# Kernel optimization log

Measured on AMD Instinct MI355X. Metric: run time of the kernel, lower is better.

## Reference

```python
import jax, jax.numpy as jnp
import numpy as np

N_HEADS = 16
EPS = 1e-4


def setup_inputs() -> dict:
    key = jax.random.key(0)
    ks = jax.random.split(key, 9)
    B, L, E = 4, 4096, 1024
    s = 1.0 / np.sqrt(E)
    return {
        "x": jax.random.normal(ks[0], (B, L, E), dtype=jnp.float32),
        "Wq": jax.random.normal(ks[1], (E, E), dtype=jnp.float32) * s,
        "bq": jax.random.normal(ks[2], (E,), dtype=jnp.float32) * 0.01,
        "Wk": jax.random.normal(ks[3], (E, E), dtype=jnp.float32) * s,
        "bk": jax.random.normal(ks[4], (E,), dtype=jnp.float32) * 0.01,
        "Wv": jax.random.normal(ks[5], (E, E), dtype=jnp.float32) * s,
        "bv": jax.random.normal(ks[6], (E,), dtype=jnp.float32) * 0.01,
        "Wo": jax.random.normal(ks[7], (E, E), dtype=jnp.float32) * s,
        "bo": jax.random.normal(ks[8], (E,), dtype=jnp.float32) * 0.01,
    }


def _cosformer(x, Wq, bq, Wk, bk, Wv, bv, Wo, bo):
    B, L, E = x.shape
    H = N_HEADS
    hd = E // H
    # torch Linear: y = x @ W.T + b; self-attention so q=k=v source is x
    q = jax.nn.relu(jnp.einsum('ble,fe->blf', x, Wq) + bq)
    k = jax.nn.relu(jnp.einsum('ble,fe->blf', x, Wk) + bk)
    v = jnp.einsum('ble,fe->blf', x, Wv) + bv
    # (B, L, E) -> (B*H, L, hd)  [matches torch view(L, B*H, hd).transpose(0,1)]
    def split_heads(t):
        return t.reshape(B, L, H, hd).transpose(0, 2, 1, 3).reshape(B * H, L, hd)
    q, k, v = split_heads(q), split_heads(k), split_heads(v)
    m = L  # src_len == tgt_len
    idx = (np.pi / 2) * jnp.arange(1, m + 1, dtype=jnp.float32) / m  # (m,)
    sin = jnp.sin(idx)[None, :, None]
    cos = jnp.cos(idx)[None, :, None]
    q_ = jnp.concatenate([q * sin, q * cos], axis=-1)  # (BH, L, 2hd)
    k_ = jnp.concatenate([k * sin, k * cos], axis=-1)
    kv = jnp.einsum('nld,nlm->ndm', k_, v)             # (BH, 2hd, hd)
    z = 1.0 / jnp.maximum(jnp.einsum('nld,nd->nl', q_, k_.sum(axis=1)), EPS)
    attn = jnp.einsum('nld,ndm->nlm', q_, kv) * z[:, :, None]  # (BH, L, hd)
    # (B*H, L, hd) -> (B, L, E)
    out = attn.reshape(B, H, L, hd).transpose(0, 2, 1, 3).reshape(B, L, E)
    return jnp.einsum('ble,fe->blf', out, Wo) + bo


def reference(x, Wq, bq, Wk, bk, Wv, bv, Wo, bo):
    return _cosformer(x, Wq, bq, Wk, bk, Wv, bv, Wo, bo)
```

## Files before the change

### kernel.cpp

```cpp
#include <hip/hip_runtime.h>


typedef unsigned short u16;
typedef unsigned int u32;
typedef __attribute__((ext_vector_type(8))) __bf16 bf16x8;
typedef __attribute__((ext_vector_type(4))) float f32x4;

#define PI_HALF 1.57079632679489662f
#define EPS_Z 1e-4f

__device__ __forceinline__ u16 f32_to_bf16(float f) {
    union { float f; unsigned int u; } x; x.f = f;
    unsigned int lsb = (x.u >> 16) & 1u;
    x.u += 0x7fffu + lsb;
    return (u16)(x.u >> 16);
}
__device__ __forceinline__ float bf16_to_f32(u16 u) {
    union { float f; unsigned int u; } x; x.u = ((unsigned int)u) << 16;
    return x.f;
}

typedef __attribute__((address_space(1))) void amdgpu_global_t;
typedef __attribute__((address_space(3))) void amdgpu_lds_t;
__device__ __forceinline__ void async_load16(const u16* g, u16* l) {
    __builtin_amdgcn_global_load_lds((amdgpu_global_t*)g, (amdgpu_lds_t*)l, 16, 0, 0);
}

__global__ __launch_bounds__(256) void cvt_bf16(const float* __restrict__ in,
                                                u16* __restrict__ out, int n4) {
    int i = blockIdx.x * 256 + threadIdx.x;
    if (i >= n4) return;
    float4 f = ((const float4*)in)[i];
    ushort4 o;
    o.x = f32_to_bf16(f.x); o.y = f32_to_bf16(f.y);
    o.z = f32_to_bf16(f.z); o.w = f32_to_bf16(f.w);
    ((ushort4*)out)[i] = o;
}

__global__ __launch_bounds__(256) void cvt_w4(const float* __restrict__ w0,
                                              const float* __restrict__ w1,
                                              const float* __restrict__ w2,
                                              const float* __restrict__ w3,
                                              u16* __restrict__ wcat) {
    const float* src = (blockIdx.y == 0) ? w0 : (blockIdx.y == 1) ? w1
                     : (blockIdx.y == 2) ? w2 : w3;
    u16* dst = wcat + (size_t)blockIdx.y * 1048576;
    int i = blockIdx.x * 256 + threadIdx.x;
    float4 f = ((const float4*)src)[i];
    ushort4 o;
    o.x = f32_to_bf16(f.x); o.y = f32_to_bf16(f.y);
    o.z = f32_to_bf16(f.z); o.w = f32_to_bf16(f.w);
    ((ushort4*)dst)[i] = o;
}

__global__ __launch_bounds__(256) void gemm_qkv(const u16* __restrict__ A,
                                                const u16* __restrict__ Wcat,
                                                const float* __restrict__ bq,
                                                const float* __restrict__ bk,
                                                const float* __restrict__ bv,
                                                u16* __restrict__ qo,
                                                u16* __restrict__ ko,
                                                u16* __restrict__ vo) {
    __shared__ u16 As[128 * 32];
    __shared__ u16 Bs[128 * 32];
    const int K = 1024;
    const int tid  = threadIdx.x;
    const int wave = tid >> 6;
    const int lane = tid & 63;
    const int quad = lane >> 4;
    const int l15  = lane & 15;
    const long tileM = (long)blockIdx.x * 128;
    const long tileN = (long)blockIdx.y * 128;
    const int mat = blockIdx.y >> 3;
    const float* bias = (mat == 0) ? bq : (mat == 1) ? bk : bv;
    u16* outp = (mat == 0) ? qo : (mat == 1) ? ko : vo;
    const bool relu = (mat < 2);
    const int wm = (wave >> 1) * 64;
    const int wn = (wave & 1) * 64;
    const int s_row = wave * 32 + (lane >> 2);
    const int s_col = (lane & 3) * 8;

    const u16* gA = A    + (tileM + s_row) * (long)K + s_col;
    const u16* gB = Wcat + (tileN + s_row) * (long)K + s_col;
    u16* lA = &As[wave * 1024];
    u16* lB = &Bs[wave * 1024];

    f32x4 acc[4][4] = {};

    for (int kb = 0; kb < K; kb += 32) {
        async_load16(gA,                lA);
        async_load16(gA + 16 * (long)K, lA + 512);
        async_load16(gB,                lB);
        async_load16(gB + 16 * (long)K, lB + 512);
        gA += 32; gB += 32;
        __syncthreads();
        bf16x8 af[4], bf[4];
#pragma unroll
        for (int i = 0; i < 4; i++) {
            af[i] = *(const bf16x8*)&As[(wm + i * 16 + l15) * 32 + quad * 8];
            bf[i] = *(const bf16x8*)&Bs[(wn + i * 16 + l15) * 32 + quad * 8];
        }
#pragma unroll
        for (int i = 0; i < 4; i++)
#pragma unroll
            for (int j = 0; j < 4; j++)
                acc[i][j] = __builtin_amdgcn_mfma_f32_16x16x32_bf16(
                    af[i], bf[j], acc[i][j], 0, 0, 0);
        __syncthreads();
    }

#pragma unroll
    for (int j = 0; j < 4; j++) {
        const long n = tileN + wn + j * 16 + l15;
        const int nl = (int)n & 1023;
        const float bv_ = bias[nl];
#pragma unroll
        for (int i = 0; i < 4; i++) {
            const long m0 = tileM + wm + i * 16 + quad * 4;
#pragma unroll
            for (int r = 0; r < 4; r++) {
                float v = acc[i][j][r] + bv_;
                if (relu) v = fmaxf(v, 0.0f);
                outp[(m0 + r) * 1024 + nl] = f32_to_bf16(v);
            }
        }
    }
}

__global__ __launch_bounds__(256) void gemm_o(const u16* __restrict__ A,
                                              const u16* __restrict__ Bw,
                                              const float* __restrict__ bias,
                                              float* __restrict__ Cout,
                                              int M, int N, int K) {
    __shared__ u16 As[128 * 32];
    __shared__ u16 Bs[128 * 32];
    const int tid  = threadIdx.x;
    const int wave = tid >> 6;
    const int lane = tid & 63;
    const int quad = lane >> 4;
    const int l15  = lane & 15;
    const long tileM = (long)blockIdx.x * 128;
    const long tileN = (long)blockIdx.y * 128;
    const int wm = (wave >> 1) * 64;
    const int wn = (wave & 1) * 64;
    const int s_row = wave * 32 + (lane >> 2);
    const int s_col = (lane & 3) * 8;

    const u16* gA = A  + (tileM + s_row) * (long)K + s_col;
    const u16* gB = Bw + (tileN + s_row) * (long)K + s_col;
    u16* lA = &As[wave * 1024];
    u16* lB = &Bs[wave * 1024];

    f32x4 acc[4][4] = {};

    for (int kb = 0; kb < K; kb += 32) {
        async_load16(gA,                lA);
        async_load16(gA + 16 * (long)K, lA + 512);
        async_load16(gB,                lB);
        async_load16(gB + 16 * (long)K, lB + 512);
        gA += 32; gB += 32;
        __syncthreads();
        bf16x8 af[4], bf[4];
#pragma unroll
        for (int i = 0; i < 4; i++) {
            af[i] = *(const bf16x8*)&As[(wm + i * 16 + l15) * 32 + quad * 8];
            bf[i] = *(const bf16x8*)&Bs[(wn + i * 16 + l15) * 32 + quad * 8];
        }
#pragma unroll
        for (int i = 0; i < 4; i++)
#pragma unroll
            for (int j = 0; j < 4; j++)
                acc[i][j] = __builtin_amdgcn_mfma_f32_16x16x32_bf16(
                    af[i], bf[j], acc[i][j], 0, 0, 0);
        __syncthreads();
    }

#pragma unroll
    for (int j = 0; j < 4; j++) {
        const long n = tileN + wn + j * 16 + l15;
        const float bv = bias[n];
#pragma unroll
        for (int i = 0; i < 4; i++) {
            const long m0 = tileM + wm + i * 16 + quad * 4;
#pragma unroll
            for (int r = 0; r < 4; r++)
                Cout[(m0 + r) * (long)N + n] = acc[i][j][r] + bv;
        }
    }
}

__global__ __launch_bounds__(256) void kv_accum(const u16* __restrict__ kmat,
                                                const u16* __restrict__ vmat,
                                                u16* __restrict__ kvp,
                                                float* __restrict__ ksp) {
    __shared__ __align__(16) float ks[32][68];
    __shared__ __align__(16) float vs[32][68];
    __shared__ float scs[32], scc[32];
    const int tid = threadIdx.x;
    const int head = blockIdx.y;
    const int b = head >> 4, h = head & 15;
    const int l0 = blockIdx.x * 128;
    const int lt = tid >> 3;
    const int g  = tid & 7;
    const int dp = tid & 31;
    const int mg = tid >> 5;
    const int dk0 = dp * 2;

    float as0[8] = {}, ac0[8] = {}, as1[8] = {}, ac1[8] = {};
    float ks0s = 0.f, ks0c = 0.f, ks1s = 0.f, ks1c = 0.f;

    for (int tile = 0; tile < 4; tile++) {
        const int lbase = l0 + tile * 32;
        {
            const long row = ((long)b * 4096 + lbase + lt) * 1024 + h * 64 + g * 8;
            uint4 kk = *(const uint4*)(kmat + row);
            uint4 vv = *(const uint4*)(vmat + row);
            const u16* kp = (const u16*)&kk;
            const u16* vp = (const u16*)&vv;
#pragma unroll
            for (int j = 0; j < 8; j++) {
                ks[lt][g * 8 + j] = bf16_to_f32(kp[j]);
                vs[lt][g * 8 + j] = bf16_to_f32(vp[j]);
            }
        }
        if (tid < 32) {
            float idx = PI_HALF * (float)(lbase + tid + 1) * (1.0f / 4096.0f);
            scs[tid] = sinf(idx);
            scc[tid] = cosf(idx);
        }
        __syncthreads();
#pragma unroll 4
        for (int l = 0; l < 32; l++) {
            const float sn = scs[l], cs = scc[l];
            const float2 kk = *(const float2*)&ks[l][dk0];
            const float k0s = kk.x * sn, k0c = kk.x * cs;
            const float k1s = kk.y * sn, k1c = kk.y * cs;
            ks0s += k0s; ks0c += k0c; ks1s += k1s; ks1c += k1c;
            const float4 va = *(const float4*)&vs[l][mg * 8];
            const float4 vb = *(const float4*)&vs[l][mg * 8 + 4];
            const float vv8[8] = {va.x, va.y, va.z, va.w, vb.x, vb.y, vb.z, vb.w};
#pragma unroll
            for (int j = 0; j < 8; j++) {
                as0[j] = fmaf(k0s, vv8[j], as0[j]);
                ac0[j] = fmaf(k0c, vv8[j], ac0[j]);
                as1[j] = fmaf(k1s, vv8[j], as1[j]);
                ac1[j] = fmaf(k1c, vv8[j], ac1[j]);
            }
        }
        __syncthreads();
    }
    u16* base = kvp + ((long)blockIdx.x * 64 + head) * 8192;
#pragma unroll
    for (int j = 0; j < 8; j++) {
        u32 s01 = (u32)f32_to_bf16(as0[j]) | ((u32)f32_to_bf16(as1[j]) << 16);
        u32 c01 = (u32)f32_to_bf16(ac0[j]) | ((u32)f32_to_bf16(ac1[j]) << 16);
        *(u32*)(base + (mg * 8 + j) * 128 + dk0)      = s01;
        *(u32*)(base + (mg * 8 + j) * 128 + 64 + dk0) = c01;
    }
    if (mg == 0) {
        float* kb2 = ksp + ((long)blockIdx.x * 64 + head) * 128;
        *(float2*)(kb2 + dk0)      = make_float2(ks0s, ks1s);
        *(float2*)(kb2 + 64 + dk0) = make_float2(ks0c, ks1c);
    }
}

__global__ __launch_bounds__(256) void kv_reduce(const u16* __restrict__ kvp,
                                                 const float* __restrict__ ksp,
                                                 u16* __restrict__ Bt) {
    const int idx = blockIdx.x * 256 + threadIdx.x;
    const int d2 = idx & 127;
    const int n  = (idx >> 7) % 80;
    const int head = idx / (80 * 128);
    float s = 0.0f;
    if (n < 64) {
#pragma unroll
        for (int c = 0; c < 32; c++)
            s += bf16_to_f32(kvp[((long)c * 64 + head) * 8192 + n * 128 + d2]);
    } else if (n == 64) {
#pragma unroll
        for (int c = 0; c < 32; c++)
            s += ksp[((long)c * 64 + head) * 128 + d2];
    }
    Bt[(long)head * 10240 + n * 128 + d2] = f32_to_bf16(s);
}

__global__ __launch_bounds__(256) void attn_mfma(const u16* __restrict__ qb,
                                                 const u16* __restrict__ Bt,
                                                 u16* __restrict__ merged) {
    __shared__ __align__(16) u16 As[128 * 72];
    __shared__ __align__(16) u16 Bs[80 * 136];
    const int tid = threadIdx.x;
    const int wave = tid >> 6, lane = tid & 63;
    const int quad = lane >> 4, l15 = lane & 15;
    const int head = blockIdx.y;
    const int b = head >> 4, h = head & 15;
    const int tm = blockIdx.x * 128;
    const long b4 = (long)b * 4096;

    for (int c = tid; c < 1024; c += 256) {
        const int row = c >> 3, c8 = c & 7;
        uint4 t = *(const uint4*)(qb + (b4 + tm + row) * 1024 + h * 64 + c8 * 8);
        *(uint4*)&As[row * 72 + c8 * 8] = t;
    }
    for (int c = tid; c < 1280; c += 256) {
        const int row = c >> 4, c16 = c & 15;
        uint4 t = *(const uint4*)(Bt + (long)head * 10240 + row * 128 + c16 * 8);
        *(uint4*)&Bs[row * 136 + c16 * 8] = t;
    }
    const int wm = wave * 32;
    float snl[2], csl[2];
#pragma unroll
    for (int i = 0; i < 2; i++) {
        const int l = tm + wm + i * 16 + l15;
        const float idx = PI_HALF * (float)(l + 1) * (1.0f / 4096.0f);
        snl[i] = sinf(idx); csl[i] = cosf(idx);
    }
    __syncthreads();

    f32x4 acc[2][5] = {};
#pragma unroll
    for (int kb = 0; kb < 4; kb++) {
        const int qc = (kb & 1) * 32 + quad * 8;
        bf16x8 af[2];
#pragma unroll
        for (int i = 0; i < 2; i++) {
            bf16x8 raw = *(const bf16x8*)&As[(wm + i * 16 + l15) * 72 + qc];
            const float s = (kb < 2) ? snl[i] : csl[i];
            bf16x8 sc;
#pragma unroll
            for (int e = 0; e < 8; e++) sc[e] = (__bf16)((float)raw[e] * s);
            af[i] = sc;
        }
        bf16x8 bf[5];
#pragma unroll
        for (int j = 0; j < 5; j++)
            bf[j] = *(const bf16x8*)&Bs[(j * 16 + l15) * 136 + kb * 32 + quad * 8];
#pragma unroll
        for (int i = 0; i < 2; i++)
#pragma unroll
            for (int j = 0; j < 5; j++)
                acc[i][j] = __builtin_amdgcn_mfma_f32_16x16x32_bf16(
                    af[i], bf[j], acc[i][j], 0, 0, 0);
    }

#pragma unroll
    for (int i = 0; i < 2; i++) {
        float z[4];
#pragma unroll
        for (int r = 0; r < 4; r++) {
            const float den = __shfl(acc[i][4][r], lane & 0x30, 64);
            z[r] = 1.0f / fmaxf(den, EPS_Z);
        }
#pragma unroll
        for (int j = 0; j < 4; j++)
#pragma unroll
            for (int r = 0; r < 4; r++) {
                const int l = tm + wm + i * 16 + quad * 4 + r;
                merged[(b4 + l) * 1024 + h * 64 + j * 16 + l15] =
                    f32_to_bf16(acc[i][j][r] * z[r]);
            }
    }
}

extern "C" void kernel_launch(void* const* d_in, const int* in_sizes, int n_in,
                              void* d_out, int out_size, void* d_ws, size_t ws_size,
                              hipStream_t stream) {
    (void)in_sizes; (void)n_in; (void)out_size; (void)ws_size;
    const float* x  = (const float*)d_in[0];
    const float* Wq = (const float*)d_in[1];
    const float* bq = (const float*)d_in[2];
    const float* Wk = (const float*)d_in[3];
    const float* bk = (const float*)d_in[4];
    const float* Wv = (const float*)d_in[5];
    const float* bv = (const float*)d_in[6];
    const float* Wo = (const float*)d_in[7];
    const float* bo = (const float*)d_in[8];
    float* out = (float*)d_out;

    const int M = 16384, E = 1024;
    char* ws = (char*)d_ws;
    const size_t MB = 1048576;
    u16* xb   = (u16*)(ws);
    u16* qb   = (u16*)(ws + 32 * MB);
    u16* kb   = (u16*)(ws + 64 * MB);
    u16* vb   = (u16*)(ws + 96 * MB);
    u16* wcat = (u16*)(ws + 128 * MB);
    u16* wob  = wcat + 3 * (size_t)E * E;
    u16* Btb  = (u16*)(ws + 136 * MB);
    float* ksp = (float*)(ws + 136 * MB + 1310720 + 2048);
    u16* kvp  = xb;
    u16* mergedb = kb;

    cvt_bf16<<<dim3(M * E / 4 / 256), dim3(256), 0, stream>>>(x, xb, M * E / 4);
    cvt_w4<<<dim3(E * E / 4 / 256, 4), dim3(256), 0, stream>>>(Wq, Wk, Wv, Wo, wcat);

    gemm_qkv<<<dim3(M / 128, 24), dim3(256), 0, stream>>>(xb, wcat, bq, bk, bv,
                                                          qb, kb, vb);

    kv_accum<<<dim3(32, 64), dim3(256), 0, stream>>>(kb, vb, kvp, ksp);
    kv_reduce<<<dim3(2560), dim3(256), 0, stream>>>(kvp, ksp, Btb);
    attn_mfma<<<dim3(32, 64), dim3(256), 0, stream>>>(qb, Btb, mergedb);

    gemm_o<<<dim3(M / 128, E / 128), dim3(256), 0, stream>>>(mergedb, wob, bo,
                                                             out, M, E, E);
}
```

Measured before the change: 410.7 us.

## Compute K^T V accumulation with bf16 MFMA and fold k-sum into ones column

Replaces the scalar-FMA kv_accum kernel with an MFMA-based kernel that transposes K and V tiles into swizzled LDS, scales K by sin/cos (updated by angle-addition recurrence), and multiplies with V plus a ones column to get the k-sum at the same time. Each block now covers 512 positions instead of 128, so there are fewer partials, which are written in fp32 and reduced by a new transposing kernel through LDS. This targets the FMA-bound kv accumulation and the reduce traffic. In exchange, scaled K is rounded to bf16 before the MFMA and the sin/cos recurrence can drift.

```diff
diff --git a/kernel.cpp b/kernel.cpp
--- a/kernel.cpp
+++ b/kernel.cpp
@@ -189,99 +189,117 @@
     }
 }
 
-__global__ __launch_bounds__(256) void kv_accum(const u16* __restrict__ kmat,
-                                                const u16* __restrict__ vmat,
-                                                u16* __restrict__ kvp,
-                                                float* __restrict__ ksp) {
-    __shared__ __align__(16) float ks[32][68];
-    __shared__ __align__(16) float vs[32][68];
-    __shared__ float scs[32], scc[32];
+__global__ __launch_bounds__(256) void kv_mfma(const u16* __restrict__ kmat,
+                                               const u16* __restrict__ vmat,
+                                               float* __restrict__ part) {
+    __shared__ u16 Ak[64 * 40];
+    __shared__ u16 Bv[64 * 40];
     const int tid = threadIdx.x;
+    const int wave = tid >> 6, lane = tid & 63;
+    const int quad = lane >> 4, l15 = lane & 15;
     const int head = blockIdx.y;
     const int b = head >> 4, h = head & 15;
-    const int l0 = blockIdx.x * 128;
-    const int lt = tid >> 3;
-    const int g  = tid & 7;
-    const int dp = tid & 31;
-    const int mg = tid >> 5;
-    const int dk0 = dp * 2;
-
-    float as0[8] = {}, ac0[8] = {}, as1[8] = {}, ac1[8] = {};
-    float ks0s = 0.f, ks0c = 0.f, ks1s = 0.f, ks1c = 0.f;
-
-    for (int tile = 0; tile < 4; tile++) {
-        const int lbase = l0 + tile * 32;
-        {
-            const long row = ((long)b * 4096 + lbase + lt) * 1024 + h * 64 + g * 8;
-            uint4 kk = *(const uint4*)(kmat + row);
-            uint4 vv = *(const uint4*)(vmat + row);
-            const u16* kp = (const u16*)&kk;
-            const u16* vp = (const u16*)&vv;
-#pragma unroll
-            for (int j = 0; j < 8; j++) {
-                ks[lt][g * 8 + j] = bf16_to_f32(kp[j]);
-                vs[lt][g * 8 + j] = bf16_to_f32(vp[j]);
-            }
-        }
-        if (tid < 32) {
-            float idx = PI_HALF * (float)(lbase + tid + 1) * (1.0f / 4096.0f);
-            scs[tid] = sinf(idx);
-            scc[tid] = cosf(idx);
-        }
-        __syncthreads();
-#pragma unroll 4
-        for (int l = 0; l < 32; l++) {
-            const float sn = scs[l], cs = scc[l];
-            const float2 kk = *(const float2*)&ks[l][dk0];
-            const float k0s = kk.x * sn, k0c = kk.x * cs;
-            const float k1s = kk.y * sn, k1c = kk.y * cs;
-            ks0s += k0s; ks0c += k0c; ks1s += k1s; ks1c += k1c;
-            const float4 va = *(const float4*)&vs[l][mg * 8];
-            const float4 vb = *(const float4*)&vs[l][mg * 8 + 4];
-            const float vv8[8] = {va.x, va.y, va.z, va.w, vb.x, vb.y, vb.z, vb.w};
-#pragma unroll
-            for (int j = 0; j < 8; j++) {
-                as0[j] = fmaf(k0s, vv8[j], as0[j]);
-                ac0[j] = fmaf(k0c, vv8[j], ac0[j]);
-                as1[j] = fmaf(k1s, vv8[j], as1[j]);
-                ac1[j] = fmaf(k1c, vv8[j], ac1[j]);
-            }
-        }
-        __syncthreads();
-    }
-    u16* base = kvp + ((long)blockIdx.x * 64 + head) * 8192;
-#pragma unroll
-    for (int j = 0; j < 8; j++) {
-        u32 s01 = (u32)f32_to_bf16(as0[j]) | ((u32)f32_to_bf16(as1[j]) << 16);
-        u32 c01 = (u32)f32_to_bf16(ac0[j]) | ((u32)f32_to_bf16(ac1[j]) << 16);
-        *(u32*)(base + (mg * 8 + j) * 128 + dk0)      = s01;
-        *(u32*)(base + (mg * 8 + j) * 128 + 64 + dk0) = c01;
-    }
-    if (mg == 0) {
-        float* kb2 = ksp + ((long)blockIdx.x * 64 + head) * 128;
-        *(float2*)(kb2 + dk0)      = make_float2(ks0s, ks1s);
-        *(float2*)(kb2 + 64 + dk0) = make_float2(ks0c, ks1c);
-    }
-}
-
-__global__ __launch_bounds__(256) void kv_reduce(const u16* __restrict__ kvp,
-                                                 const float* __restrict__ ksp,
-                                                 u16* __restrict__ Bt) {
-    const int idx = blockIdx.x * 256 + threadIdx.x;
-    const int d2 = idx & 127;
-    const int n  = (idx >> 7) % 80;
-    const int head = idx / (80 * 128);
-    float s = 0.0f;
-    if (n < 64) {
-#pragma unroll
-        for (int c = 0; c < 32; c++)
-            s += bf16_to_f32(kvp[((long)c * 64 + head) * 8192 + n * 128 + d2]);
-    } else if (n == 64) {
-#pragma unroll
-        for (int c = 0; c < 32; c++)
-            s += ksp[((long)c * 64 + head) * 128 + d2];
-    }
-    Bt[(long)head * 10240 + n * 128 + d2] = f32_to_bf16(s);
+    const int l0 = blockIdx.x * 512;
+    const int sl = tid >> 3;
+    const int sc8 = tid & 7;
+    const int scol = sl ^ ((sc8 & 3) << 3);
+    const int krow_base = (wave & 1) * 32;
+    const bool use_cos = (wave >> 1) != 0;
+    const int mbase = wave * 32;
+
+    float sv[8], cv[8];
+#pragma unroll
+    for (int e = 0; e < 8; e++) {
+        float ang = (PI_HALF / 4096.0f) * (float)(l0 + quad * 8 + e + 1);
+        sv[e] = sinf(ang); cv[e] = cosf(ang);
+    }
+    const float cD = 0.9999247018391445f;
+    const float sD = 0.0122715382857199f;
+
+    bf16x8 onesf;
+#pragma unroll
+    for (int e = 0; e < 8; e++)
+        onesf[e] = (l15 == 0) ? (__bf16)1.0f : (__bf16)0.0f;
+
+    f32x4 acc[2][5] = {};
+
+    for (int kt = 0; kt < 16; kt++) {
+        const long row = ((long)b * 4096 + l0 + kt * 32 + sl) * 1024 + h * 64 + sc8 * 8;
+        uint4 kk = *(const uint4*)(kmat + row);
+        uint4 vv = *(const uint4*)(vmat + row);
+        const u16* kp = (const u16*)&kk;
+        const u16* vp = (const u16*)&vv;
+#pragma unroll
+        for (int e = 0; e < 8; e++) {
+            const int d = sc8 * 8 + e;
+            Ak[d * 40 + scol] = kp[e];
+            Bv[d * 40 + scol] = vp[e];
+        }
+        __syncthreads();
+
+        bf16x8 af[2];
+#pragma unroll
+        for (int i = 0; i < 2; i++) {
+            const int d = krow_base + i * 16 + l15;
+            const int q2 = (quad ^ ((d >> 3) & 3)) * 8;
+            bf16x8 raw = *(const bf16x8*)&Ak[d * 40 + q2];
+            bf16x8 sc;
+#pragma unroll
+            for (int e = 0; e < 8; e++)
+                sc[e] = (__bf16)((float)raw[e] * (use_cos ? cv[e] : sv[e]));
+            af[i] = sc;
+        }
+        bf16x8 bfr[5];
+#pragma unroll
+        for (int j = 0; j < 4; j++) {
+            const int n = j * 16 + l15;
+            const int q2 = (quad ^ ((n >> 3) & 3)) * 8;
+            bfr[j] = *(const bf16x8*)&Bv[n * 40 + q2];
+        }
+        bfr[4] = onesf;
+#pragma unroll
+        for (int i = 0; i < 2; i++)
+#pragma unroll
+            for (int j = 0; j < 5; j++)
+                acc[i][j] = __builtin_amdgcn_mfma_f32_16x16x32_bf16(
+                    af[i], bfr[j], acc[i][j], 0, 0, 0);
+
+#pragma unroll
+        for (int e = 0; e < 8; e++) {
+            const float ns = sv[e] * cD + cv[e] * sD;
+            cv[e] = cv[e] * cD - sv[e] * sD;
+            sv[e] = ns;
+        }
+        __syncthreads();
+    }
+
+    float* op = part + ((long)blockIdx.x * 64 + head) * 10240;
+#pragma unroll
+    for (int i = 0; i < 2; i++)
+#pragma unroll
+        for (int j = 0; j < 5; j++)
+#pragma unroll
+            for (int r = 0; r < 4; r++)
+                op[(mbase + i * 16 + quad * 4 + r) * 80 + j * 16 + l15] = acc[i][j][r];
+}
+
+__global__ __launch_bounds__(256) void kv_reduce_t(const float* __restrict__ part,
+                                                   u16* __restrict__ Bt) {
+    __shared__ float accs[32 * 81];
+    const int head = blockIdx.y, d2t = blockIdx.x;
+    const float* bp = part + (long)head * 10240 + d2t * 32 * 80;
+    for (int idx = threadIdx.x; idx < 2560; idx += 256) {
+        float s = 0.0f;
+#pragma unroll
+        for (int c = 0; c < 8; c++) s += bp[(long)c * 655360 + idx];
+        const int d2 = idx / 80, n = idx - d2 * 80;
+        accs[d2 * 81 + n] = s;
+    }
+    __syncthreads();
+    for (int idx = threadIdx.x; idx < 2560; idx += 256) {
+        const int n = idx >> 5, d2 = idx & 31;
+        Bt[(long)head * 10240 + n * 128 + d2t * 32 + d2] = f32_to_bf16(accs[d2 * 81 + n]);
+    }
 }
 
 __global__ __launch_bounds__(256) void attn_mfma(const u16* __restrict__ qb,
@@ -387,8 +405,7 @@
     u16* wcat = (u16*)(ws + 128 * MB);
     u16* wob  = wcat + 3 * (size_t)E * E;
     u16* Btb  = (u16*)(ws + 136 * MB);
-    float* ksp = (float*)(ws + 136 * MB + 1310720 + 2048);
-    u16* kvp  = xb;
+    float* part = (float*)xb;
     u16* mergedb = kb;
 
     cvt_bf16<<<dim3(M * E / 4 / 256), dim3(256), 0, stream>>>(x, xb, M * E / 4);
@@ -397,8 +414,8 @@
     gemm_qkv<<<dim3(M / 128, 24), dim3(256), 0, stream>>>(xb, wcat, bq, bk, bv,
                                                           qb, kb, vb);
 
-    kv_accum<<<dim3(32, 64), dim3(256), 0, stream>>>(kb, vb, kvp, ksp);
-    kv_reduce<<<dim3(2560), dim3(256), 0, stream>>>(kvp, ksp, Btb);
+    kv_mfma<<<dim3(8, 64), dim3(256), 0, stream>>>(kb, vb, part);
+    kv_reduce_t<<<dim3(4, 64), dim3(256), 0, stream>>>(part, Btb);
     attn_mfma<<<dim3(32, 64), dim3(256), 0, stream>>>(qb, Btb, mergedb);
 
     gemm_o<<<dim3(M / 128, E / 128), dim3(256), 0, stream>>>(mergedb, wob, bo,
```

After: 384.0 us. 6.5% less time.
